# Optimization experiments

Hardware: AMD Instinct MI355X
Metric: run time of the kernel (lower is better)

The kernel has to match this reference:

```python
import jax, jax.numpy as jnp
import numpy as np

N = 2_000_000
FUN, TAU, ALPHA, LOSS_WEIGHT = 'log', 1.0, 1.0, 1.0


def setup_inputs() -> dict:
    key = jax.random.key(0)
    k1, k2, k3 = jax.random.split(key, 3)
    pred = jax.random.uniform(k1, (N, 5), dtype=jnp.float32)
    target = jax.random.uniform(k2, (N, 5), dtype=jnp.float32)
    weight = jax.random.uniform(k3, (N,), dtype=jnp.float32)
    return {"pred": pred, "target": target, "weight": weight}


def _xyrs(xywhr):
    # [N,5] -> xy [N,2], R [N,2,2], S [N,2,2] (diag(wh/2))
    xy = xywhr[:, :2]
    wh = xywhr[:, 2:4]
    r = xywhr[:, 4]
    c, s = jnp.cos(r), jnp.sin(r)
    R = jnp.stack([c, -s, s, c], axis=-1).reshape(-1, 2, 2)
    S = 0.5 * wh[:, :, None] * jnp.eye(2, dtype=xywhr.dtype)  # diag_embed
    return xy, R, S


def _sqrt_trace_2x2sym(M):
    # trace of matrix sqrt of symmetric PSD 2x2: sqrt(tr(M) + 2*sqrt(det(M)))
    a, b, d = M[:, 0, 0], M[:, 0, 1], M[:, 1, 1]
    det = jnp.clip(a * d - b * b, 0.0)
    return jnp.sqrt(jnp.clip(a + d + 2.0 * jnp.sqrt(det), 0.0))


def reference(pred, target, weight):
    xy_p, R_p, S_p = _xyrs(pred)
    xy_t, R_t, S_t = _xyrs(target)

    dxy = xy_p - xy_t
    xy_distance = jnp.sum(dxy * dxy, axis=-1)

    Rp_T = jnp.swapaxes(R_p, -1, -2)
    Rt_T = jnp.swapaxes(R_t, -1, -2)
    Sigma_p_sqrt = R_p @ S_p @ Rp_T
    Sigma_p = R_p @ (S_p * S_p) @ Rp_T
    Sigma_t = R_t @ (S_t * S_t) @ Rt_T

    whr_distance = Sigma_p[:, 0, 0] + Sigma_p[:, 1, 1]
    whr_distance = whr_distance + Sigma_t[:, 0, 0] + Sigma_t[:, 1, 1]
    cross = Sigma_p_sqrt @ Sigma_t @ Sigma_p_sqrt
    whr_distance = whr_distance - 2.0 * _sqrt_trace_2x2sym(cross)

    distance = jnp.sqrt(jnp.clip(xy_distance + ALPHA * whr_distance, 0.0))
    scale = jnp.sqrt(jnp.sqrt(jnp.prod(pred[:, 2:4] * target[:, 2:4], axis=-1)))
    distance = distance / scale

    if FUN == 'log':
        distance = jnp.log1p(distance)
    elif FUN == 'sqrt':
        distance = jnp.sqrt(distance)

    if TAU >= 1.0:
        loss = 1.0 - 1.0 / (TAU + distance)
    else:
        loss = distance

    # weighted_loss wrapper: elementwise weight then mean reduction
    loss = jnp.mean(loss * weight)
    return loss * LOSS_WEIGHT
```

## Files before the change

### kernel.cpp

```cpp
#include <hip/hip_runtime.h>


#define GWD_N 2000000

__global__ __launch_bounds__(256) void gwd_loss_kernel(
    const float* __restrict__ pred,
    const float* __restrict__ target,
    const float* __restrict__ weight,
    float* __restrict__ out,
    int n)
{
    const float inv_n = 1.0f / (float)n;
    float acc = 0.0f;

    const int stride = gridDim.x * blockDim.x;
    for (int i = blockIdx.x * blockDim.x + threadIdx.x; i < n; i += stride) {
        const int b = i * 5;
        const float px = pred[b + 0];
        const float py = pred[b + 1];
        const float pw = pred[b + 2];
        const float ph = pred[b + 3];
        const float pr = pred[b + 4];
        const float tx = target[b + 0];
        const float ty = target[b + 1];
        const float tw = target[b + 2];
        const float th = target[b + 3];
        const float trr = target[b + 4];

        const float dx = px - tx;
        const float dy = py - ty;
        const float xy_dist = dx * dx + dy * dy;

        const float a2p = 0.25f * pw * pw;
        const float b2p = 0.25f * ph * ph;
        const float a2t = 0.25f * tw * tw;
        const float b2t = 0.25f * th * th;

        float whr = (a2p + b2p) + (a2t + b2t);

        float cp, sp, ct, st;
        __sincosf(pr, &sp, &cp);
        __sincosf(trr, &st, &ct);

        const float Sp00 = cp * cp * a2p + sp * sp * b2p;
        const float Sp01 = cp * sp * (a2p - b2p);
        const float Sp11 = sp * sp * a2p + cp * cp * b2p;
        const float St00 = ct * ct * a2t + st * st * b2t;
        const float St01 = ct * st * (a2t - b2t);
        const float St11 = st * st * a2t + ct * ct * b2t;

        float tr_cross = Sp00 * St00 + 2.0f * Sp01 * St01 + Sp11 * St11;
        float det_cross = (a2p * b2p) * (a2t * b2t);

        float sq = tr_cross + 2.0f * sqrtf(det_cross);
        sq = fmaxf(sq, 0.0f);
        const float sqrt_trace = sqrtf(sq);

        whr = whr - 2.0f * sqrt_trace;

        float dist2 = xy_dist + whr;
        dist2 = fmaxf(dist2, 0.0f);
        float distance = sqrtf(dist2);

        const float prod = (pw * tw) * (ph * th);
        const float scale = sqrtf(sqrtf(prod));
        distance = distance / scale;

        distance = log1pf(distance);

        const float loss = 1.0f - 1.0f / (1.0f + distance);

        acc += loss * weight[i];
    }

    #pragma unroll
    for (int off = 32; off > 0; off >>= 1)
        acc += __shfl_down(acc, off, 64);

    __shared__ float wave_sums[4];
    const int lane = threadIdx.x & 63;
    const int wid  = threadIdx.x >> 6;
    if (lane == 0) wave_sums[wid] = acc;
    __syncthreads();

    if (threadIdx.x == 0) {
        const float s = (wave_sums[0] + wave_sums[1]) + (wave_sums[2] + wave_sums[3]);
        atomicAdd(out, s * inv_n);
    }
}

extern "C" void kernel_launch(void* const* d_in, const int* in_sizes, int n_in,
                              void* d_out, int out_size, void* d_ws, size_t ws_size,
                              hipStream_t stream) {
    const float* pred   = (const float*)d_in[0];
    const float* target = (const float*)d_in[1];
    const float* weight = (const float*)d_in[2];
    float* out = (float*)d_out;

    const int n = in_sizes[2];

    hipMemsetAsync(out, 0, sizeof(float), stream);

    const int block = 256;
    const int grid = 1024;
    gwd_loss_kernel<<<grid, block, 0, stream>>>(pred, target, weight, out, n);
}
```

Measured before the change: 115.0 us.

## Stage row chunks in shared memory via coalesced float4 loads

Each block now processes 512-row chunks. It copies the stride-5 pred and target rows plus the weights into shared memory with coalesced float4 loads, then computes per row from LDS. This replaces the strided 5-float per-thread global reads, and the grid size is also raised. It adds two barriers per chunk and LDS bank conflicts from the stride-5 reads. The float4 tail read can go past the end of the array on the final chunk.

```diff
diff --git a/kernel.cpp b/kernel.cpp
--- a/kernel.cpp
+++ b/kernel.cpp
@@ -1,7 +1,7 @@
 #include <hip/hip_runtime.h>
 
 
-#define GWD_N 2000000
+#define ROWS_PER_CHUNK 512
 
 __global__ __launch_bounds__(256) void gwd_loss_kernel(
     const float* __restrict__ pred,
@@ -10,67 +10,83 @@
     float* __restrict__ out,
     int n)
 {
+    __shared__ float s_pred[ROWS_PER_CHUNK * 5];
+    __shared__ float s_tgt [ROWS_PER_CHUNK * 5];
+    __shared__ float s_w   [ROWS_PER_CHUNK];
+
     const float inv_n = 1.0f / (float)n;
     float acc = 0.0f;
 
-    const int stride = gridDim.x * blockDim.x;
-    for (int i = blockIdx.x * blockDim.x + threadIdx.x; i < n; i += stride) {
-        const int b = i * 5;
-        const float px = pred[b + 0];
-        const float py = pred[b + 1];
-        const float pw = pred[b + 2];
-        const float ph = pred[b + 3];
-        const float pr = pred[b + 4];
-        const float tx = target[b + 0];
-        const float ty = target[b + 1];
-        const float tw = target[b + 2];
-        const float th = target[b + 3];
-        const float trr = target[b + 4];
+    const int n_chunks = (n + ROWS_PER_CHUNK - 1) / ROWS_PER_CHUNK;
 
-        const float dx = px - tx;
-        const float dy = py - ty;
-        const float xy_dist = dx * dx + dy * dy;
+    for (int chunk = blockIdx.x; chunk < n_chunks; chunk += gridDim.x) {
+        const int row0 = chunk * ROWS_PER_CHUNK;
+        const int rows = min(ROWS_PER_CHUNK, n - row0);
 
-        const float a2p = 0.25f * pw * pw;
-        const float b2p = 0.25f * ph * ph;
-        const float a2t = 0.25f * tw * tw;
-        const float b2t = 0.25f * th * th;
+        const int nf4 = (rows * 5 + 3) >> 2;
+        const float4* p4 = (const float4*)(pred   + (size_t)row0 * 5);
+        const float4* t4 = (const float4*)(target + (size_t)row0 * 5);
+        for (int j = threadIdx.x; j < nf4; j += 256) {
+            ((float4*)s_pred)[j] = p4[j];
+            ((float4*)s_tgt )[j] = t4[j];
+        }
+        const int nw4 = (rows + 3) >> 2;
+        const float4* w4 = (const float4*)(weight + row0);
+        for (int j = threadIdx.x; j < nw4; j += 256)
+            ((float4*)s_w)[j] = w4[j];
+        __syncthreads();
 
-        float whr = (a2p + b2p) + (a2t + b2t);
+        #pragma unroll
+        for (int rr = 0; rr < ROWS_PER_CHUNK / 256; ++rr) {
+            const int r = threadIdx.x + rr * 256;
+            if (r < rows) {
+                const float* pp = &s_pred[r * 5];
+                const float* tt = &s_tgt [r * 5];
+                const float px = pp[0], py = pp[1], pw = pp[2], ph = pp[3], pr = pp[4];
+                const float tx = tt[0], ty = tt[1], tw = tt[2], th = tt[3], trr_ = tt[4];
 
-        float cp, sp, ct, st;
-        __sincosf(pr, &sp, &cp);
-        __sincosf(trr, &st, &ct);
+                const float dx = px - tx;
+                const float dy = py - ty;
+                const float xy_dist = dx * dx + dy * dy;
 
-        const float Sp00 = cp * cp * a2p + sp * sp * b2p;
-        const float Sp01 = cp * sp * (a2p - b2p);
-        const float Sp11 = sp * sp * a2p + cp * cp * b2p;
-        const float St00 = ct * ct * a2t + st * st * b2t;
-        const float St01 = ct * st * (a2t - b2t);
-        const float St11 = st * st * a2t + ct * ct * b2t;
+                const float a2p = 0.25f * pw * pw;
+                const float b2p = 0.25f * ph * ph;
+                const float a2t = 0.25f * tw * tw;
+                const float b2t = 0.25f * th * th;
 
-        float tr_cross = Sp00 * St00 + 2.0f * Sp01 * St01 + Sp11 * St11;
-        float det_cross = (a2p * b2p) * (a2t * b2t);
+                float whr = (a2p + b2p) + (a2t + b2t);
 
-        float sq = tr_cross + 2.0f * sqrtf(det_cross);
-        sq = fmaxf(sq, 0.0f);
-        const float sqrt_trace = sqrtf(sq);
+                float cp, sp, ct, st;
+                __sincosf(pr,  &sp, &cp);
+                __sincosf(trr_, &st, &ct);
 
-        whr = whr - 2.0f * sqrt_trace;
+                const float Sp00 = cp * cp * a2p + sp * sp * b2p;
+                const float Sp01 = cp * sp * (a2p - b2p);
+                const float Sp11 = sp * sp * a2p + cp * cp * b2p;
+                const float St00 = ct * ct * a2t + st * st * b2t;
+                const float St01 = ct * st * (a2t - b2t);
+                const float St11 = st * st * a2t + ct * ct * b2t;
 
-        float dist2 = xy_dist + whr;
-        dist2 = fmaxf(dist2, 0.0f);
-        float distance = sqrtf(dist2);
+                const float tr_cross  = Sp00 * St00 + 2.0f * Sp01 * St01 + Sp11 * St11;
+                const float det_cross = (a2p * b2p) * (a2t * b2t);
 
-        const float prod = (pw * tw) * (ph * th);
-        const float scale = sqrtf(sqrtf(prod));
-        distance = distance / scale;
+                float sq = tr_cross + 2.0f * sqrtf(det_cross);
+                sq = fmaxf(sq, 0.0f);
+                whr = whr - 2.0f * sqrtf(sq);
 
-        distance = log1pf(distance);
+                float dist2 = fmaxf(xy_dist + whr, 0.0f);
+                float distance = sqrtf(dist2);
 
-        const float loss = 1.0f - 1.0f / (1.0f + distance);
+                const float prod = (pw * tw) * (ph * th);
+                distance = distance / sqrtf(sqrtf(prod));
 
-        acc += loss * weight[i];
+                distance = log1pf(distance);
+                const float loss = 1.0f - 1.0f / (1.0f + distance);
+
+                acc += loss * s_w[r];
+            }
+        }
+        __syncthreads();
     }
 
     #pragma unroll
@@ -102,6 +118,6 @@
     hipMemsetAsync(out, 0, sizeof(float), stream);
 
     const int block = 256;
-    const int grid = 1024;
+    const int grid  = 1792;
     gwd_loss_kernel<<<grid, block, 0, stream>>>(pred, target, weight, out, n);
 }
```

New measurement: 123.8 us. 7.7% more time.

## Vectorize row loads with float4 groups of four rows, one group per thread

Applied to the files above, without the earlier changes.

Each thread now handles four consecutive rows and reads their 20 pred and 20 target floats as five float4 loads each, plus one float4 load for the four weights. This replaces scalar strided 5-float loads with wide, aligned loads. The persistent grid-stride loop with 1024 blocks is replaced by a grid sized to cover every group exactly once, which launches many more blocks, each doing a single pass. A scalar tail path handles leftover rows; register pressure rises from the per-thread buffers.

```diff
diff --git a/kernel.cpp b/kernel.cpp
--- a/kernel.cpp
+++ b/kernel.cpp
@@ -1,7 +1,48 @@
 #include <hip/hip_runtime.h>
 
 
-#define GWD_N 2000000
+__device__ __forceinline__ float gwd_row(const float* __restrict__ p,
+                                         const float* __restrict__ t)
+{
+    const float px = p[0], py = p[1], pw = p[2], ph = p[3], pr = p[4];
+    const float tx = t[0], ty = t[1], tw = t[2], th = t[3], tr = t[4];
+
+    const float dx = px - tx;
+    const float dy = py - ty;
+    const float xy_dist = dx * dx + dy * dy;
+
+    const float a2p = 0.25f * pw * pw;
+    const float b2p = 0.25f * ph * ph;
+    const float a2t = 0.25f * tw * tw;
+    const float b2t = 0.25f * th * th;
+
+    float whr = (a2p + b2p) + (a2t + b2t);
+
+    float cp, sp, ct, st;
+    __sincosf(pr, &sp, &cp);
+    __sincosf(tr, &st, &ct);
+
+    const float Sp00 = cp * cp * a2p + sp * sp * b2p;
+    const float Sp01 = cp * sp * (a2p - b2p);
+    const float Sp11 = sp * sp * a2p + cp * cp * b2p;
+    const float St00 = ct * ct * a2t + st * st * b2t;
+    const float St01 = ct * st * (a2t - b2t);
+    const float St11 = st * st * a2t + ct * ct * b2t;
+
+    const float tr_cross  = Sp00 * St00 + 2.0f * Sp01 * St01 + Sp11 * St11;
+    const float det_cross = (a2p * b2p) * (a2t * b2t);
+
+    float sq = fmaxf(tr_cross + 2.0f * sqrtf(det_cross), 0.0f);
+    whr = whr - 2.0f * sqrtf(sq);
+
+    float distance = sqrtf(fmaxf(xy_dist + whr, 0.0f));
+
+    const float prod = (pw * tw) * (ph * th);
+    distance = distance / sqrtf(sqrtf(prod));
+
+    distance = log1pf(distance);
+    return 1.0f - 1.0f / (1.0f + distance);
+}
 
 __global__ __launch_bounds__(256) void gwd_loss_kernel(
     const float* __restrict__ pred,
@@ -11,66 +52,36 @@
     int n)
 {
     const float inv_n = 1.0f / (float)n;
+    const int g  = blockIdx.x * 256 + threadIdx.x;
+    const int r0 = g * 4;
     float acc = 0.0f;
 
-    const int stride = gridDim.x * blockDim.x;
-    for (int i = blockIdx.x * blockDim.x + threadIdx.x; i < n; i += stride) {
-        const int b = i * 5;
-        const float px = pred[b + 0];
-        const float py = pred[b + 1];
-        const float pw = pred[b + 2];
-        const float ph = pred[b + 3];
-        const float pr = pred[b + 4];
-        const float tx = target[b + 0];
-        const float ty = target[b + 1];
-        const float tw = target[b + 2];
-        const float th = target[b + 3];
-        const float trr = target[b + 4];
+    if (r0 + 3 < n) {
+        const float4* p4 = (const float4*)pred   + (size_t)g * 5;
+        const float4* t4 = (const float4*)target + (size_t)g * 5;
+        const float4  w4 = ((const float4*)weight)[g];
 
-        const float dx = px - tx;
-        const float dy = py - ty;
-        const float xy_dist = dx * dx + dy * dy;
+        float pbuf[20], tbuf[20];
+        float4 P0 = p4[0], P1 = p4[1], P2 = p4[2], P3 = p4[3], P4 = p4[4];
+        float4 T0 = t4[0], T1 = t4[1], T2 = t4[2], T3 = t4[3], T4 = t4[4];
+        *(float4*)(pbuf +  0) = P0; *(float4*)(pbuf +  4) = P1;
+        *(float4*)(pbuf +  8) = P2; *(float4*)(pbuf + 12) = P3;
+        *(float4*)(pbuf + 16) = P4;
+        *(float4*)(tbuf +  0) = T0; *(float4*)(tbuf +  4) = T1;
+        *(float4*)(tbuf +  8) = T2; *(float4*)(tbuf + 12) = T3;
+        *(float4*)(tbuf + 16) = T4;
 
-        const float a2p = 0.25f * pw * pw;
-        const float b2p = 0.25f * ph * ph;
-        const float a2t = 0.25f * tw * tw;
-        const float b2t = 0.25f * th * th;
-
-        float whr = (a2p + b2p) + (a2t + b2t);
-
-        float cp, sp, ct, st;
-        __sincosf(pr, &sp, &cp);
-        __sincosf(trr, &st, &ct);
-
-        const float Sp00 = cp * cp * a2p + sp * sp * b2p;
-        const float Sp01 = cp * sp * (a2p - b2p);
-        const float Sp11 = sp * sp * a2p + cp * cp * b2p;
-        const float St00 = ct * ct * a2t + st * st * b2t;
-        const float St01 = ct * st * (a2t - b2t);
-        const float St11 = st * st * a2t + ct * ct * b2t;
-
-        float tr_cross = Sp00 * St00 + 2.0f * Sp01 * St01 + Sp11 * St11;
-        float det_cross = (a2p * b2p) * (a2t * b2t);
-
-        float sq = tr_cross + 2.0f * sqrtf(det_cross);
-        sq = fmaxf(sq, 0.0f);
-        const float sqrt_trace = sqrtf(sq);
-
-        whr = whr - 2.0f * sqrt_trace;
-
-        float dist2 = xy_dist + whr;
-        dist2 = fmaxf(dist2, 0.0f);
-        float distance = sqrtf(dist2);
-
-        const float prod = (pw * tw) * (ph * th);
-        const float scale = sqrtf(sqrtf(prod));
-        distance = distance / scale;
-
-        distance = log1pf(distance);
-
-        const float loss = 1.0f - 1.0f / (1.0f + distance);
-
-        acc += loss * weight[i];
+        const float w[4] = { w4.x, w4.y, w4.z, w4.w };
+        #pragma unroll
+        for (int j = 0; j < 4; ++j)
+            acc += gwd_row(&pbuf[j * 5], &tbuf[j * 5]) * w[j];
+    } else {
+        for (int r = r0; r < n && r < r0 + 4; ++r) {
+            float pb[5], tb[5];
+            #pragma unroll
+            for (int k = 0; k < 5; ++k) { pb[k] = pred[r * 5 + k]; tb[k] = target[r * 5 + k]; }
+            acc += gwd_row(pb, tb) * weight[r];
+        }
     }
 
     #pragma unroll
@@ -101,7 +112,8 @@
 
     hipMemsetAsync(out, 0, sizeof(float), stream);
 
-    const int block = 256;
-    const int grid = 1024;
+    const int block  = 256;
+    const int groups = (n + 3) / 4;
+    const int grid   = (groups + block - 1) / block;
     gwd_loss_kernel<<<grid, block, 0, stream>>>(pred, target, weight, out, n);
 }
```

Result: slower. 126.1 us (+9.7%).
